# Optimization experiments

Measured on AMD Instinct MI355X. Metric: run time of the kernel, lower is better.

The kernel has to match this reference:

```python
import jax, jax.numpy as jnp
import numpy as np

B, N, C, K, OUT = 2, 8192, 64, 20, 64
EDGE_DIM = C * 3 + 5  # 197
BN_EPS = 1e-5


def setup_inputs() -> dict:
    key = jax.random.key(0)
    k1, k2 = jax.random.split(key, 2)
    x = jax.random.normal(k1, (B, C, N), jnp.float32)
    conv_w = jax.random.normal(k2, (OUT, EDGE_DIM), jnp.float32) * 0.05
    return {
        "x": x,
        "conv_w": conv_w,
        "bn_gamma": jnp.ones((OUT,), jnp.float32),
        "bn_beta": jnp.zeros((OUT,), jnp.float32),
        "bn_mean": jnp.zeros((OUT,), jnp.float32),
        "bn_var": jnp.ones((OUT,), jnp.float32),
        "k": K,
    }


def reference(x, conv_w, bn_gamma, bn_beta, bn_mean, bn_var, k):
    xt = jnp.transpose(x, (0, 2, 1))          # [B, N, C]
    b, n, c = xt.shape
    xyz = xt[:, :, :3]                         # [B, N, 3]

    # ---- kNN on xyz (negative squared distance, top-k) ----
    inner = -2.0 * jnp.matmul(xyz, jnp.transpose(xyz, (0, 2, 1)))  # [B,N,N]
    xx = jnp.sum(xyz * xyz, axis=2, keepdims=True)                 # [B,N,1]
    pd = -xx - inner - jnp.transpose(xx, (0, 2, 1))                # [B,N,N]
    _, idx = jax.lax.top_k(pd, k)                                  # [B,N,k]

    # ---- gather neighbors ----
    neighbors = jax.vmap(lambda xi, ii: xi[ii])(xt, idx)           # [B,N,k,C]
    x_ctr = xt[:, :, None, :]                                      # [B,N,1,C]
    base = jnp.concatenate(
        [jnp.broadcast_to(x_ctr, (b, n, k, c)), neighbors - x_ctr, neighbors],
        axis=3)                                                    # [B,N,k,3C]

    # ---- geometric features ----
    xyz_nb = neighbors[:, :, :, :3]
    vec = xyz_nb - xyz[:, :, None, :]                              # [B,N,k,3]
    dist = jnp.linalg.norm(vec, axis=3, keepdims=True)             # [B,N,k,1]
    local_density = jnp.broadcast_to(dist.mean(axis=2, keepdims=True), dist.shape)
    z_ctr = xyz[:, :, 2:3]                                         # [B,N,1]
    z_nb = xyz_nb[:, :, :, 2:3]                                    # [B,N,k,1]
    rel_h = jnp.broadcast_to(z_ctr[:, :, None, :] - z_nb.mean(axis=2, keepdims=True), dist.shape)
    dist_var = jnp.broadcast_to(jnp.var(dist, axis=2, keepdims=True, ddof=1), dist.shape)
    vn = vec / (dist + 1e-6)
    md = vn.mean(axis=2, keepdims=True)
    md = md / (jnp.linalg.norm(md, axis=3, keepdims=True) + 1e-6)
    cos = jnp.sum(vn * md, axis=3, keepdims=True)
    angle = 1.0 - jnp.abs(cos)

    edge = jnp.concatenate([base, dist, local_density, rel_h, dist_var, angle], axis=3)  # [B,N,k,EDGE_DIM]

    # ---- 1x1 conv + BN (inference stats) + LeakyReLU(0.2) + max over neighbors ----
    y = jnp.einsum('bnkf,of->bnko', edge, conv_w)                  # [B,N,k,OUT]
    scale = bn_gamma / jnp.sqrt(bn_var + BN_EPS)
    y = (y - bn_mean) * scale + bn_beta
    y = jnp.where(y >= 0, y, 0.2 * y)
    out = y.max(axis=2)                                            # [B,N,OUT]
    return jnp.transpose(out, (0, 2, 1))                           # [B,OUT,N]
```

## Files before the change

kernel.cpp:

```cpp
#include <hip/hip_runtime.h>


#define NPTS 8192
#define NBATCH 2
#define NQ (NBATCH * NPTS)
#define CH 64
#define KNN 20
#define EDIM 197
#define QW 4
#define KWAVES 16
#define QB (QW * KWAVES)
#define CAPC 64

__device__ __forceinline__ float wsum(float v) {
  v += __shfl_xor(v, 1, 64);
  v += __shfl_xor(v, 2, 64);
  v += __shfl_xor(v, 4, 64);
  v += __shfl_xor(v, 8, 64);
  v += __shfl_xor(v, 16, 64);
  v += __shfl_xor(v, 32, 64);
  return v;
}

__device__ __forceinline__ float dtilde(float m2x, float m2y, float m2z, float4 c) {
  return fmaf(m2x, c.x, fmaf(m2y, c.y, fmaf(m2z, c.z, c.w)));
}

__device__ __forceinline__ double d2d(float qx, float qy, float qz, float4 c) {
  double dx = (double)qx - (double)c.x;
  double dy = (double)qy - (double)c.y;
  double dz = (double)qz - (double)c.z;
  return dx * dx + dy * dy + dz * dz;
}

__device__ __forceinline__ float bcastf(float v, int l) {
  return __int_as_float(__builtin_amdgcn_readlane(__float_as_int(v), l));
}

__global__ __launch_bounds__(256) void prep_kernel(const float* __restrict__ x,
                                                   const float* __restrict__ w,
                                                   float4* __restrict__ cpack,
                                                   float* __restrict__ wprep) {
  int t = blockIdx.x * 256 + threadIdx.x;
  if (t < NQ) {
    int b = t >> 13, n = t & (NPTS - 1);
    const float* xb = x + (size_t)b * CH * NPTS;
    float cx = xb[n], cy = xb[NPTS + n], cz = xb[2 * NPTS + n];
    cpack[t] = make_float4(cx, cy, cz, fmaf(cx, cx, fmaf(cy, cy, cz * cz)));
  }
  if (t < 2 * CH * CH) {
    int mat = t >> 12, c = (t >> 6) & 63, o = t & 63;
    float w1 = w[o * EDIM + c];
    float w2 = w[o * EDIM + 64 + c];
    float w3 = w[o * EDIM + 128 + c];
    wprep[t] = mat ? (w2 + w3) : (w1 - w2);
  }
}

__global__ __launch_bounds__(256) void proj_kernel(const float* __restrict__ x,
                                                   const float* __restrict__ wprep,
                                                   float* __restrict__ projc,
                                                   float* __restrict__ projn) {
  __shared__ float wl[CH * 16];
  int by = blockIdx.y;
  int mat = by >> 2, oq = by & 3;
  for (int i = threadIdx.x; i < CH * 16; i += 256) {
    int c = i >> 4, oo = i & 15;
    wl[i] = wprep[mat * CH * CH + c * CH + oq * 16 + oo];
  }
  __syncthreads();
  int p = blockIdx.x * 256 + threadIdx.x;
  int b = p >> 13, n = p & (NPTS - 1);
  const float* xb = x + (size_t)b * CH * NPTS + n;
  float acc[16];
#pragma unroll
  for (int o = 0; o < 16; ++o) acc[o] = 0.f;
#pragma unroll 4
  for (int c = 0; c < CH; ++c) {
    float xv = xb[(size_t)c * NPTS];
    const float4* wr = (const float4*)(wl + c * 16);
#pragma unroll
    for (int o4 = 0; o4 < 4; ++o4) {
      float4 wv = wr[o4];
      acc[o4 * 4 + 0] = fmaf(wv.x, xv, acc[o4 * 4 + 0]);
      acc[o4 * 4 + 1] = fmaf(wv.y, xv, acc[o4 * 4 + 1]);
      acc[o4 * 4 + 2] = fmaf(wv.z, xv, acc[o4 * 4 + 2]);
      acc[o4 * 4 + 3] = fmaf(wv.w, xv, acc[o4 * 4 + 3]);
    }
  }
  float* dst = (mat ? projn : projc) + (size_t)p * 64 + oq * 16;
#pragma unroll
  for (int o4 = 0; o4 < 4; ++o4)
    ((float4*)dst)[o4] = make_float4(acc[o4 * 4 + 0], acc[o4 * 4 + 1],
                                     acc[o4 * 4 + 2], acc[o4 * 4 + 3]);
}

__global__ __launch_bounds__(1024) void knnfeat_kernel(const float4* __restrict__ cpack,
                                                       const float* __restrict__ projc,
                                                       const float* __restrict__ projn,
                                                       const float* __restrict__ w,
                                                       const float* __restrict__ gamma,
                                                       const float* __restrict__ beta,
                                                       const float* __restrict__ mean,
                                                       const float* __restrict__ var,
                                                       float* __restrict__ out) {
  __shared__ float4 t4[NPTS];
  __shared__ int lidx[KWAVES][QW][CAPC];
  __shared__ int nsel[KWAVES][QW][KNN];
  int tid = threadIdx.x;
  int lane = tid & 63;
  int wq = tid >> 6;
  int blk = blockIdx.x;
  int bb = blk >> 7;
  int q0 = blk * QB + wq * QW;
  const float4* cb = cpack + bb * NPTS;

  for (int i = tid; i < NPTS; i += 1024) t4[i] = cb[i];
  float qx[QW], qy[QW], qz[QW], m2x[QW], m2y[QW], m2z[QW];
#pragma unroll
  for (int qi = 0; qi < QW; ++qi) {
    float4 qp = cpack[q0 + qi];
    qx[qi] = qp.x; qy[qi] = qp.y; qz[qi] = qp.z;
    m2x[qi] = -2.f * qp.x; m2y[qi] = -2.f * qp.y; m2z[qi] = -2.f * qp.z;
  }
  __syncthreads();

  float m[QW];
#pragma unroll
  for (int qi = 0; qi < QW; ++qi) m[qi] = 3.0e38f;
#pragma unroll 2
  for (int i = 0; i < NPTS / 64; ++i) {
    float4 c = t4[lane + i * 64];
#pragma unroll
    for (int qi = 0; qi < QW; ++qi)
      m[qi] = fminf(m[qi], dtilde(m2x[qi], m2y[qi], m2z[qi], c));
  }
  float lo[QW], hi[QW];
#pragma unroll
  for (int qi = 0; qi < QW; ++qi) { lo[qi] = -512.f; hi[qi] = 512.f; }
#pragma unroll 1
  for (int it = 0; it < 28; ++it) {
#pragma unroll
    for (int qi = 0; qi < QW; ++qi) {
      float mid = (lo[qi] + hi[qi]) * 0.5f;
      int c = (int)__popcll(__ballot(m[qi] <= mid));
      if (c >= KNN) hi[qi] = mid; else lo[qi] = mid;
    }
  }

  int cnt[QW];
#pragma unroll
  for (int qi = 0; qi < QW; ++qi) cnt[qi] = 0;
  unsigned long long lmlt = (1ull << lane) - 1ull;
#pragma unroll 2
  for (int i = 0; i < NPTS / 64; ++i) {
    float4 c = t4[lane + i * 64];
#pragma unroll
    for (int qi = 0; qi < QW; ++qi) {
      bool pr = dtilde(m2x[qi], m2y[qi], m2z[qi], c) <= hi[qi];
      unsigned long long mk = __ballot(pr);
      if (mk) {
        int ofs = cnt[qi] + (int)__popcll(mk & lmlt);
        if (pr && ofs < CAPC) lidx[wq][qi][ofs] = lane + i * 64;
        cnt[qi] += (int)__popcll(mk);
      }
    }
  }

  double dd[QW]; int ii[QW];
#pragma unroll
  for (int qi = 0; qi < QW; ++qi) {
    int C = min(cnt[qi], CAPC);
    dd[qi] = 1e300; ii[qi] = -1;
    if (lane < C) {
      int id = lidx[wq][qi][lane];
      dd[qi] = d2d(qx[qi], qy[qi], qz[qi], t4[id]);
      ii[qi] = id;
    }
  }
#pragma unroll
  for (int qi = 0; qi < QW; ++qi) {
    int C = min(cnt[qi], CAPC);
    int xlo = __double2loint(dd[qi]), xhi = __double2hiint(dd[qi]);
    int r = 0;
#pragma unroll 1
    for (int j = 0; j < C; ++j) {
      double dj = __hiloint2double(__builtin_amdgcn_readlane(xhi, j),
                                   __builtin_amdgcn_readlane(xlo, j));
      int idj = __builtin_amdgcn_readlane(ii[qi], j);
      r += (dj < dd[qi]) || (dj == dd[qi] && idj < ii[qi]);
    }
    if (ii[qi] >= 0 && r < KNN) nsel[wq][qi][r] = ii[qi];
  }

  float* zbuf = (float*)&lidx[0][0][0];
  float wd  = w[lane * EDIM + 192];
  float wld = w[lane * EDIM + 193];
  float wrh = w[lane * EDIM + 194];
  float wdv = w[lane * EDIM + 195];
  float wa  = w[lane * EDIM + 196];
  float sc = gamma[lane] / sqrtf(var[lane] + 1e-5f);
  float muv = mean[lane], bt = beta[lane];
#pragma unroll 1
  for (int qi = 0; qi < QW; ++qi) {
    int gq = q0 + qi;
    int jj = nsel[wq][qi][lane < KNN ? lane : 0] & (NPTS - 1);
    float4 nb = t4[jj];
    float vx = nb.x - qx[qi], vy = nb.y - qy[qi], vz = nb.z - qz[qi];
    float dist = sqrtf(fmaf(vx, vx, fmaf(vy, vy, vz * vz)));
    float inv = 1.f / (dist + 1e-6f);
    float vnx = vx * inv, vny = vy * inv, vnz = vz * inv;
    float msk = (lane < KNN) ? 1.f : 0.f;
    float sd = wsum(dist * msk);
    float szn = wsum(nb.z * msk);
    float sx = wsum(vnx * msk);
    float sy = wsum(vny * msk);
    float s3 = wsum(vnz * msk);
    float ld = sd * (1.f / KNN);
    float rh = qz[qi] - szn * (1.f / KNN);
    float dev = dist - ld;
    float dvs = wsum(dev * dev * msk);
    float dv = dvs * (1.f / (KNN - 1));
    float mdx = sx * (1.f / KNN), mdy = sy * (1.f / KNN), mdz = s3 * (1.f / KNN);
    float mnorm = sqrtf(fmaf(mdx, mdx, fmaf(mdy, mdy, mdz * mdz)));
    float rinv = 1.f / (mnorm + 1e-6f);
    mdx *= rinv; mdy *= rinv; mdz *= rinv;
    float cosv = vnx * mdx + vny * mdy + vnz * mdz;
    float angle = 1.f - fabsf(cosv);
    float base = projc[(size_t)gq * 64 + lane] + ld * wld + rh * wrh + dv * wdv;
    float zmax = -3.0e38f, zmin = 3.0e38f;
#pragma unroll
    for (int kk = 0; kk < KNN; ++kk) {
      float dk = bcastf(dist, kk);
      float ak = bcastf(angle, kk);
      int jk = __builtin_amdgcn_readlane(jj, kk);
      float z = base + projn[(size_t)(bb * NPTS + jk) * 64 + lane] + dk * wd + ak * wa;
      zmax = fmaxf(zmax, z);
      zmin = fminf(zmin, z);
    }
    float M = (sc >= 0.f) ? zmax : zmin;
    float yv = (M - muv) * sc + bt;
    yv = (yv >= 0.f) ? yv : 0.2f * yv;
    int qcol = wq * QW + qi;
    zbuf[qcol * 64 + ((lane + qcol) & 63)] = yv;
  }
  __syncthreads();
  {
    int o = tid >> 4, g = tid & 15;
    int n0 = (blk & 127) * 64;
    int q4 = g * 4;
    float4 v;
    v.x = zbuf[(q4 + 0) * 64 + ((o + q4 + 0) & 63)];
    v.y = zbuf[(q4 + 1) * 64 + ((o + q4 + 1) & 63)];
    v.z = zbuf[(q4 + 2) * 64 + ((o + q4 + 2) & 63)];
    v.w = zbuf[(q4 + 3) * 64 + ((o + q4 + 3) & 63)];
    *(float4*)(out + (size_t)bb * CH * NPTS + (size_t)o * NPTS + n0 + q4) = v;
  }
}

extern "C" void kernel_launch(void* const* d_in, const int* in_sizes, int n_in,
                              void* d_out, int out_size, void* d_ws, size_t ws_size,
                              hipStream_t stream) {
  const float* x = (const float*)d_in[0];
  const float* w = (const float*)d_in[1];
  const float* gamma = (const float*)d_in[2];
  const float* beta = (const float*)d_in[3];
  const float* mean = (const float*)d_in[4];
  const float* var = (const float*)d_in[5];
  float* out = (float*)d_out;

  const size_t OFF_CPACK = 0;
  const size_t OFF_WPREP = 262144;
  const size_t OFF_PROJC = 294912;
  const size_t OFF_PROJN = 294912 + 4194304;
  const size_t NEED = 294912 + 8388608;
  if (ws_size < NEED) return;

  char* ws = (char*)d_ws;
  float4* cpack = (float4*)(ws + OFF_CPACK);
  float* wprep = (float*)(ws + OFF_WPREP);
  float* projc = (float*)(ws + OFF_PROJC);
  float* projn = (float*)(ws + OFF_PROJN);

  prep_kernel<<<64, 256, 0, stream>>>(x, w, cpack, wprep);
  proj_kernel<<<dim3(64, 8), 256, 0, stream>>>(x, wprep, projc, projn);
  knnfeat_kernel<<<256, 1024, 0, stream>>>(cpack, projc, projn, w,
                                           gamma, beta, mean, var, out);
}
```

Before: 83.91 us.

## Widen projection to 64 outputs per thread, use LDS atomics for candidate compaction

The projection kernel now has each thread compute all 64 outputs from a full 64x64 weight tile in shared memory, with 2 blocks in y instead of 8. This reads x once instead of four times, at the cost of much higher register use and lower occupancy. In the kNN kernel, candidate collection switches from ballot/popcount prefix compaction to per-query LDS atomic counters. The bisection range and iteration count are narrowed, and the feature loop unroll is raised. The atomics make candidate order nondeterministic, but the later rank-by-distance step sorts them anyway.

```diff
diff --git a/kernel.cpp b/kernel.cpp
--- a/kernel.cpp
+++ b/kernel.cpp
@@ -61,26 +61,22 @@
                                                    const float* __restrict__ wprep,
                                                    float* __restrict__ projc,
                                                    float* __restrict__ projn) {
-  __shared__ float wl[CH * 16];
-  int by = blockIdx.y;
-  int mat = by >> 2, oq = by & 3;
-  for (int i = threadIdx.x; i < CH * 16; i += 256) {
-    int c = i >> 4, oo = i & 15;
-    wl[i] = wprep[mat * CH * CH + c * CH + oq * 16 + oo];
-  }
+  __shared__ float wl[CH * CH];
+  int mat = blockIdx.y;
+  for (int i = threadIdx.x; i < CH * CH; i += 256) wl[i] = wprep[mat * CH * CH + i];
   __syncthreads();
   int p = blockIdx.x * 256 + threadIdx.x;
   int b = p >> 13, n = p & (NPTS - 1);
   const float* xb = x + (size_t)b * CH * NPTS + n;
-  float acc[16];
-#pragma unroll
-  for (int o = 0; o < 16; ++o) acc[o] = 0.f;
-#pragma unroll 4
+  float acc[64];
+#pragma unroll
+  for (int o = 0; o < 64; ++o) acc[o] = 0.f;
+#pragma unroll 2
   for (int c = 0; c < CH; ++c) {
     float xv = xb[(size_t)c * NPTS];
-    const float4* wr = (const float4*)(wl + c * 16);
-#pragma unroll
-    for (int o4 = 0; o4 < 4; ++o4) {
+    const float4* wr = (const float4*)(wl + c * 64);
+#pragma unroll
+    for (int o4 = 0; o4 < 16; ++o4) {
       float4 wv = wr[o4];
       acc[o4 * 4 + 0] = fmaf(wv.x, xv, acc[o4 * 4 + 0]);
       acc[o4 * 4 + 1] = fmaf(wv.y, xv, acc[o4 * 4 + 1]);
@@ -88,9 +84,9 @@
       acc[o4 * 4 + 3] = fmaf(wv.w, xv, acc[o4 * 4 + 3]);
     }
   }
-  float* dst = (mat ? projn : projc) + (size_t)p * 64 + oq * 16;
-#pragma unroll
-  for (int o4 = 0; o4 < 4; ++o4)
+  float* dst = (mat ? projn : projc) + (size_t)p * 64;
+#pragma unroll
+  for (int o4 = 0; o4 < 16; ++o4)
     ((float4*)dst)[o4] = make_float4(acc[o4 * 4 + 0], acc[o4 * 4 + 1],
                                      acc[o4 * 4 + 2], acc[o4 * 4 + 3]);
 }
@@ -107,6 +103,7 @@
   __shared__ float4 t4[NPTS];
   __shared__ int lidx[KWAVES][QW][CAPC];
   __shared__ int nsel[KWAVES][QW][KNN];
+  __shared__ int acnt[KWAVES][QW];
   int tid = threadIdx.x;
   int lane = tid & 63;
   int wq = tid >> 6;
@@ -116,6 +113,7 @@
   const float4* cb = cpack + bb * NPTS;
 
   for (int i = tid; i < NPTS; i += 1024) t4[i] = cb[i];
+  if (lane < QW) acnt[wq][lane] = 0;
   float qx[QW], qy[QW], qz[QW], m2x[QW], m2y[QW], m2z[QW];
 #pragma unroll
   for (int qi = 0; qi < QW; ++qi) {
@@ -137,9 +135,9 @@
   }
   float lo[QW], hi[QW];
 #pragma unroll
-  for (int qi = 0; qi < QW; ++qi) { lo[qi] = -512.f; hi[qi] = 512.f; }
+  for (int qi = 0; qi < QW; ++qi) { lo[qi] = -256.f; hi[qi] = 256.f; }
 #pragma unroll 1
-  for (int it = 0; it < 28; ++it) {
+  for (int it = 0; it < 24; ++it) {
 #pragma unroll
     for (int qi = 0; qi < QW; ++qi) {
       float mid = (lo[qi] + hi[qi]) * 0.5f;
@@ -148,31 +146,24 @@
     }
   }
 
-  int cnt[QW];
-#pragma unroll
-  for (int qi = 0; qi < QW; ++qi) cnt[qi] = 0;
-  unsigned long long lmlt = (1ull << lane) - 1ull;
 #pragma unroll 2
   for (int i = 0; i < NPTS / 64; ++i) {
     float4 c = t4[lane + i * 64];
 #pragma unroll
     for (int qi = 0; qi < QW; ++qi) {
-      bool pr = dtilde(m2x[qi], m2y[qi], m2z[qi], c) <= hi[qi];
-      unsigned long long mk = __ballot(pr);
-      if (mk) {
-        int ofs = cnt[qi] + (int)__popcll(mk & lmlt);
-        if (pr && ofs < CAPC) lidx[wq][qi][ofs] = lane + i * 64;
-        cnt[qi] += (int)__popcll(mk);
+      if (dtilde(m2x[qi], m2y[qi], m2z[qi], c) <= hi[qi]) {
+        int s = atomicAdd(&acnt[wq][qi], 1);
+        if (s < CAPC) lidx[wq][qi][s] = lane + i * 64;
       }
     }
   }
 
-  double dd[QW]; int ii[QW];
-#pragma unroll
-  for (int qi = 0; qi < QW; ++qi) {
-    int C = min(cnt[qi], CAPC);
+  double dd[QW]; int ii[QW]; int cC[QW];
+#pragma unroll
+  for (int qi = 0; qi < QW; ++qi) {
+    cC[qi] = min(acnt[wq][qi], CAPC);
     dd[qi] = 1e300; ii[qi] = -1;
-    if (lane < C) {
+    if (lane < cC[qi]) {
       int id = lidx[wq][qi][lane];
       dd[qi] = d2d(qx[qi], qy[qi], qz[qi], t4[id]);
       ii[qi] = id;
@@ -180,11 +171,10 @@
   }
 #pragma unroll
   for (int qi = 0; qi < QW; ++qi) {
-    int C = min(cnt[qi], CAPC);
     int xlo = __double2loint(dd[qi]), xhi = __double2hiint(dd[qi]);
     int r = 0;
 #pragma unroll 1
-    for (int j = 0; j < C; ++j) {
+    for (int j = 0; j < cC[qi]; ++j) {
       double dj = __hiloint2double(__builtin_amdgcn_readlane(xhi, j),
                                    __builtin_amdgcn_readlane(xlo, j));
       int idj = __builtin_amdgcn_readlane(ii[qi], j);
@@ -201,7 +191,7 @@
   float wa  = w[lane * EDIM + 196];
   float sc = gamma[lane] / sqrtf(var[lane] + 1e-5f);
   float muv = mean[lane], bt = beta[lane];
-#pragma unroll 1
+#pragma unroll 2
   for (int qi = 0; qi < QW; ++qi) {
     int gq = q0 + qi;
     int jj = nsel[wq][qi][lane < KNN ? lane : 0] & (NPTS - 1);
@@ -283,7 +273,7 @@
   float* projn = (float*)(ws + OFF_PROJN);
 
   prep_kernel<<<64, 256, 0, stream>>>(x, w, cpack, wprep);
-  proj_kernel<<<dim3(64, 8), 256, 0, stream>>>(x, wprep, projc, projn);
+  proj_kernel<<<dim3(64, 2), 256, 0, stream>>>(x, wprep, projc, projn);
   knnfeat_kernel<<<256, 1024, 0, stream>>>(cpack, projc, projn, w,
                                            gamma, beta, mean, var, out);
 }
```

Result: slower. 109.6 us (+30.6%).

## Fold prep into projection kernel and retile kNN to eight queries per wave

Applied to the files above, without the earlier changes.

Removes the separate prep kernel: the projection kernel now builds the combined weights from the raw conv weights and writes the packed xyz+norm buffer itself, saving one launch and a workspace round-trip. The kNN kernel moves to 512-thread blocks with 8 queries per wave, so each LDS candidate load is reused across more queries, and sets launch bounds for two blocks per CU. Several tuning changes come with it: a narrower bisection range with fewer iterations, more unrolling, and a wider output transpose store. The narrower bisection range of plus or minus 256 assumes squared distances stay in that range, and the extra per-wave queries raise register pressure.

```diff
diff --git a/kernel.cpp b/kernel.cpp
--- a/kernel.cpp
+++ b/kernel.cpp
@@ -7,8 +7,8 @@
 #define CH 64
 #define KNN 20
 #define EDIM 197
-#define QW 4
-#define KWAVES 16
+#define QW 8
+#define KWAVES 8
 #define QB (QW * KWAVES)
 #define CAPC 64
 
@@ -37,28 +37,9 @@
   return __int_as_float(__builtin_amdgcn_readlane(__float_as_int(v), l));
 }
 
-__global__ __launch_bounds__(256) void prep_kernel(const float* __restrict__ x,
+__global__ __launch_bounds__(256) void proj_kernel(const float* __restrict__ x,
                                                    const float* __restrict__ w,
                                                    float4* __restrict__ cpack,
-                                                   float* __restrict__ wprep) {
-  int t = blockIdx.x * 256 + threadIdx.x;
-  if (t < NQ) {
-    int b = t >> 13, n = t & (NPTS - 1);
-    const float* xb = x + (size_t)b * CH * NPTS;
-    float cx = xb[n], cy = xb[NPTS + n], cz = xb[2 * NPTS + n];
-    cpack[t] = make_float4(cx, cy, cz, fmaf(cx, cx, fmaf(cy, cy, cz * cz)));
-  }
-  if (t < 2 * CH * CH) {
-    int mat = t >> 12, c = (t >> 6) & 63, o = t & 63;
-    float w1 = w[o * EDIM + c];
-    float w2 = w[o * EDIM + 64 + c];
-    float w3 = w[o * EDIM + 128 + c];
-    wprep[t] = mat ? (w2 + w3) : (w1 - w2);
-  }
-}
-
-__global__ __launch_bounds__(256) void proj_kernel(const float* __restrict__ x,
-                                                   const float* __restrict__ wprep,
                                                    float* __restrict__ projc,
                                                    float* __restrict__ projn) {
   __shared__ float wl[CH * 16];
@@ -66,7 +47,11 @@
   int mat = by >> 2, oq = by & 3;
   for (int i = threadIdx.x; i < CH * 16; i += 256) {
     int c = i >> 4, oo = i & 15;
-    wl[i] = wprep[mat * CH * CH + c * CH + oq * 16 + oo];
+    int o = oq * 16 + oo;
+    float w1 = w[o * EDIM + c];
+    float w2 = w[o * EDIM + 64 + c];
+    float w3 = w[o * EDIM + 128 + c];
+    wl[i] = mat ? (w2 + w3) : (w1 - w2);
   }
   __syncthreads();
   int p = blockIdx.x * 256 + threadIdx.x;
@@ -93,17 +78,21 @@
   for (int o4 = 0; o4 < 4; ++o4)
     ((float4*)dst)[o4] = make_float4(acc[o4 * 4 + 0], acc[o4 * 4 + 1],
                                      acc[o4 * 4 + 2], acc[o4 * 4 + 3]);
-}
-
-__global__ __launch_bounds__(1024) void knnfeat_kernel(const float4* __restrict__ cpack,
-                                                       const float* __restrict__ projc,
-                                                       const float* __restrict__ projn,
-                                                       const float* __restrict__ w,
-                                                       const float* __restrict__ gamma,
-                                                       const float* __restrict__ beta,
-                                                       const float* __restrict__ mean,
-                                                       const float* __restrict__ var,
-                                                       float* __restrict__ out) {
+  if (by == 0) {
+    float cx = xb[0], cy = xb[(size_t)NPTS], cz = xb[(size_t)2 * NPTS];
+    cpack[p] = make_float4(cx, cy, cz, fmaf(cx, cx, fmaf(cy, cy, cz * cz)));
+  }
+}
+
+__global__ __launch_bounds__(512, 2) void knnfeat_kernel(const float4* __restrict__ cpack,
+                                                         const float* __restrict__ projc,
+                                                         const float* __restrict__ projn,
+                                                         const float* __restrict__ w,
+                                                         const float* __restrict__ gamma,
+                                                         const float* __restrict__ beta,
+                                                         const float* __restrict__ mean,
+                                                         const float* __restrict__ var,
+                                                         float* __restrict__ out) {
   __shared__ float4 t4[NPTS];
   __shared__ int lidx[KWAVES][QW][CAPC];
   __shared__ int nsel[KWAVES][QW][KNN];
@@ -115,7 +104,7 @@
   int q0 = blk * QB + wq * QW;
   const float4* cb = cpack + bb * NPTS;
 
-  for (int i = tid; i < NPTS; i += 1024) t4[i] = cb[i];
+  for (int i = tid; i < NPTS; i += 512) t4[i] = cb[i];
   float qx[QW], qy[QW], qz[QW], m2x[QW], m2y[QW], m2z[QW];
 #pragma unroll
   for (int qi = 0; qi < QW; ++qi) {
@@ -128,7 +117,7 @@
   float m[QW];
 #pragma unroll
   for (int qi = 0; qi < QW; ++qi) m[qi] = 3.0e38f;
-#pragma unroll 2
+#pragma unroll 4
   for (int i = 0; i < NPTS / 64; ++i) {
     float4 c = t4[lane + i * 64];
 #pragma unroll
@@ -137,9 +126,9 @@
   }
   float lo[QW], hi[QW];
 #pragma unroll
-  for (int qi = 0; qi < QW; ++qi) { lo[qi] = -512.f; hi[qi] = 512.f; }
+  for (int qi = 0; qi < QW; ++qi) { lo[qi] = -256.f; hi[qi] = 256.f; }
 #pragma unroll 1
-  for (int it = 0; it < 28; ++it) {
+  for (int it = 0; it < 24; ++it) {
 #pragma unroll
     for (int qi = 0; qi < QW; ++qi) {
       float mid = (lo[qi] + hi[qi]) * 0.5f;
@@ -167,12 +156,12 @@
     }
   }
 
-  double dd[QW]; int ii[QW];
-#pragma unroll
-  for (int qi = 0; qi < QW; ++qi) {
-    int C = min(cnt[qi], CAPC);
+  double dd[QW]; int ii[QW]; int cC[QW];
+#pragma unroll
+  for (int qi = 0; qi < QW; ++qi) {
+    cC[qi] = min(cnt[qi], CAPC);
     dd[qi] = 1e300; ii[qi] = -1;
-    if (lane < C) {
+    if (lane < cC[qi]) {
       int id = lidx[wq][qi][lane];
       dd[qi] = d2d(qx[qi], qy[qi], qz[qi], t4[id]);
       ii[qi] = id;
@@ -180,11 +169,10 @@
   }
 #pragma unroll
   for (int qi = 0; qi < QW; ++qi) {
-    int C = min(cnt[qi], CAPC);
     int xlo = __double2loint(dd[qi]), xhi = __double2hiint(dd[qi]);
     int r = 0;
 #pragma unroll 1
-    for (int j = 0; j < C; ++j) {
+    for (int j = 0; j < cC[qi]; ++j) {
       double dj = __hiloint2double(__builtin_amdgcn_readlane(xhi, j),
                                    __builtin_amdgcn_readlane(xlo, j));
       int idj = __builtin_amdgcn_readlane(ii[qi], j);
@@ -201,7 +189,7 @@
   float wa  = w[lane * EDIM + 196];
   float sc = gamma[lane] / sqrtf(var[lane] + 1e-5f);
   float muv = mean[lane], bt = beta[lane];
-#pragma unroll 1
+#pragma unroll 2
   for (int qi = 0; qi < QW; ++qi) {
     int gq = q0 + qi;
     int jj = nsel[wq][qi][lane < KNN ? lane : 0] & (NPTS - 1);
@@ -246,15 +234,21 @@
   }
   __syncthreads();
   {
-    int o = tid >> 4, g = tid & 15;
+    int o = tid >> 3, g = tid & 7;
     int n0 = (blk & 127) * 64;
-    int q4 = g * 4;
-    float4 v;
-    v.x = zbuf[(q4 + 0) * 64 + ((o + q4 + 0) & 63)];
-    v.y = zbuf[(q4 + 1) * 64 + ((o + q4 + 1) & 63)];
-    v.z = zbuf[(q4 + 2) * 64 + ((o + q4 + 2) & 63)];
-    v.w = zbuf[(q4 + 3) * 64 + ((o + q4 + 3) & 63)];
-    *(float4*)(out + (size_t)bb * CH * NPTS + (size_t)o * NPTS + n0 + q4) = v;
+    int q8 = g * 8;
+    float4 v0, v1;
+    v0.x = zbuf[(q8 + 0) * 64 + ((o + q8 + 0) & 63)];
+    v0.y = zbuf[(q8 + 1) * 64 + ((o + q8 + 1) & 63)];
+    v0.z = zbuf[(q8 + 2) * 64 + ((o + q8 + 2) & 63)];
+    v0.w = zbuf[(q8 + 3) * 64 + ((o + q8 + 3) & 63)];
+    v1.x = zbuf[(q8 + 4) * 64 + ((o + q8 + 4) & 63)];
+    v1.y = zbuf[(q8 + 5) * 64 + ((o + q8 + 5) & 63)];
+    v1.z = zbuf[(q8 + 6) * 64 + ((o + q8 + 6) & 63)];
+    v1.w = zbuf[(q8 + 7) * 64 + ((o + q8 + 7) & 63)];
+    float* op = out + (size_t)bb * CH * NPTS + (size_t)o * NPTS + n0 + q8;
+    *(float4*)op = v0;
+    *(float4*)(op + 4) = v1;
   }
 }
 
@@ -270,20 +264,17 @@
   float* out = (float*)d_out;
 
   const size_t OFF_CPACK = 0;
-  const size_t OFF_WPREP = 262144;
-  const size_t OFF_PROJC = 294912;
-  const size_t OFF_PROJN = 294912 + 4194304;
-  const size_t NEED = 294912 + 8388608;
+  const size_t OFF_PROJC = 262144;
+  const size_t OFF_PROJN = 262144 + 4194304;
+  const size_t NEED = 262144 + 8388608;
   if (ws_size < NEED) return;
 
   char* ws = (char*)d_ws;
   float4* cpack = (float4*)(ws + OFF_CPACK);
-  float* wprep = (float*)(ws + OFF_WPREP);
   float* projc = (float*)(ws + OFF_PROJC);
   float* projn = (float*)(ws + OFF_PROJN);
 
-  prep_kernel<<<64, 256, 0, stream>>>(x, w, cpack, wprep);
-  proj_kernel<<<dim3(64, 8), 256, 0, stream>>>(x, wprep, projc, projn);
-  knnfeat_kernel<<<256, 1024, 0, stream>>>(cpack, projc, projn, w,
-                                           gamma, beta, mean, var, out);
-}
+  proj_kernel<<<dim3(64, 8), 256, 0, stream>>>(x, w, cpack, projc, projn);
+  knnfeat_kernel<<<256, 512, 0, stream>>>(cpack, projc, projn, w,
+                                          gamma, beta, mean, var, out);
+}
```

Result: slower. 111.3 us (+32.7%).
